# Kernel tuning notes

Measured on AMD Instinct MI355X. Metric: run time of the kernel, lower is better.

Reference implementation:

```python
import jax, jax.numpy as jnp
import numpy as np

N, E, CIN, H, L = 50000, 800000, 128, 256, 3
EPS = 1e-5  # BatchNorm1d default eps


def setup_inputs() -> dict:
    key = jax.random.key(0)
    ks = jax.random.split(key, 24)
    x = jax.random.normal(ks[0], (N, CIN), dtype=jnp.float32)
    edge_index = jax.random.randint(ks[1], (2, E), 0, N, dtype=jnp.int64)
    params = {}
    cin = CIN
    for i in range(L):
        s = 1.0 / np.sqrt(cin).astype(np.float32)
        params[f"Wl{i}"] = jax.random.normal(ks[2 + 3 * i], (cin, H), dtype=jnp.float32) * s
        params[f"Wr{i}"] = jax.random.normal(ks[3 + 3 * i], (cin, H), dtype=jnp.float32) * s
        params[f"b{i}"] = jax.random.normal(ks[4 + 3 * i], (H,), dtype=jnp.float32) * 0.01
        cin = H
    gamma = jax.random.uniform(ks[20], (L, H), minval=0.5, maxval=1.5, dtype=jnp.float32)
    beta = jax.random.normal(ks[21], (L, H), dtype=jnp.float32) * 0.1
    rmean = jax.random.normal(ks[22], (L, H), dtype=jnp.float32) * 0.1
    rvar = jax.random.uniform(ks[23], (L, H), minval=0.5, maxval=1.5, dtype=jnp.float32)
    return dict(x=x, edge_index=edge_index, gamma=gamma, beta=beta,
                rmean=rmean, rvar=rvar, **params)


def reference(x, edge_index, gamma, beta, rmean, rvar,
              Wl0, Wr0, b0, Wl1, Wr1, b1, Wl2, Wr2, b2):
    src, dst = edge_index[0], edge_index[1]
    # in-degree of each destination node, clamped to 1 (mean aggregation)
    deg = jnp.maximum(
        jax.ops.segment_sum(jnp.ones((E,), jnp.float32), dst, num_segments=N), 1.0
    )[:, None]

    def layer(h, Wl, Wr, b, g, bt, rm, rv):
        # SAGEConv (mean): out = lin_l(mean_j x_j) + lin_r(x)
        agg = jax.ops.segment_sum(h[src], dst, num_segments=N) / deg  # [N, C]
        out = agg @ Wl + h @ Wr + b                                   # [N, H]
        # BatchNorm1d (eval mode: running stats) + ReLU; dropout is identity in eval
        out = (out - rm) * jax.lax.rsqrt(rv + EPS) * g + bt
        return jax.nn.relu(out)

    weights = [(Wl0, Wr0, b0), (Wl1, Wr1, b1), (Wl2, Wr2, b2)]
    for i, (Wl, Wr, b) in enumerate(weights):
        x = layer(x, Wl, Wr, b, gamma[i], beta[i], rmean[i], rvar[i])
    return x
```

## Files before the change

kernel.cpp:

```cpp
#include <hip/hip_runtime.h>
#include <hip/hip_bf16.h>

#define NN 50000
#define PADN 50048
#define EE 800000
#define HH 256
#define EPSBN 1e-5f
#define NBLK ((NN + 255) / 256)

typedef unsigned int uint32;
typedef __attribute__((ext_vector_type(8))) short short8;
typedef __attribute__((ext_vector_type(4))) float f32x4;
typedef __attribute__((ext_vector_type(2))) float f32x2;

__device__ __forceinline__ float bf2f(unsigned short u) {
    union { uint32 u; float f; } c; c.u = ((uint32)u) << 16; return c.f;
}
__device__ __forceinline__ unsigned short f2bf(float f) {
    __hip_bfloat16 h = __float2bfloat16(f);
    return *reinterpret_cast<unsigned short*>(&h);
}
__device__ __forceinline__ uint32 pkfp8(float a, float b, float c, float d) {
    int r = 0;
    r = __builtin_amdgcn_cvt_pk_fp8_f32(a, b, r, false);
    r = __builtin_amdgcn_cvt_pk_fp8_f32(c, d, r, true);
    return (uint32)r;
}


__global__ void cvt_x(const float* __restrict__ x, unsigned short* __restrict__ xb,
                      unsigned char* __restrict__ x8, int* __restrict__ deg) {
    int i = blockIdx.x * blockDim.x + threadIdx.x;
    if (i < NN) deg[i] = 0;
    if (i >= PADN * 128 / 8) return;
    const int e0 = i * 8;
    float f[8];
    if (e0 + 8 <= NN * 128) {
        float4 u0 = *(const float4*)(x + e0);
        float4 u1 = *(const float4*)(x + e0 + 4);
        f[0] = u0.x; f[1] = u0.y; f[2] = u0.z; f[3] = u0.w;
        f[4] = u1.x; f[5] = u1.y; f[6] = u1.z; f[7] = u1.w;
    } else {
        #pragma unroll
        for (int k = 0; k < 8; ++k) f[k] = 0.f;
    }
    uint4 b;
    b.x = (uint32)f2bf(f[0]) | ((uint32)f2bf(f[1]) << 16);
    b.y = (uint32)f2bf(f[2]) | ((uint32)f2bf(f[3]) << 16);
    b.z = (uint32)f2bf(f[4]) | ((uint32)f2bf(f[5]) << 16);
    b.w = (uint32)f2bf(f[6]) | ((uint32)f2bf(f[7]) << 16);
    *(uint4*)(xb + e0) = b;
    uint2 p;
    p.x = pkfp8(f[0], f[1], f[2], f[3]);
    p.y = pkfp8(f[4], f[5], f[6], f[7]);
    *(uint2*)(x8 + e0) = p;
}

__global__ void count_rank(const int* __restrict__ dst, int* __restrict__ deg,
                           int* __restrict__ rank) {
    int e = blockIdx.x * blockDim.x + threadIdx.x;
    if (e < EE) rank[e] = atomicAdd(&deg[dst[e]], 1);
}

__global__ void scan_part(const int* __restrict__ deg, int* __restrict__ bsum) {
    __shared__ int sd[256];
    const int t = (int)threadIdx.x;
    const int i = (int)blockIdx.x * 256 + t;
    sd[t] = (i < NN) ? deg[i] : 0;
    __syncthreads();
    #pragma unroll
    for (int off = 128; off > 0; off >>= 1) {
        if (t < off) sd[t] += sd[t + off];
        __syncthreads();
    }
    if (t == 0) bsum[blockIdx.x] = sd[0];
}

__global__ void scan_fin(const int* __restrict__ deg, const int* __restrict__ bsum,
                         int* __restrict__ rowstart) {
    __shared__ int sb[256];
    __shared__ int sd[256];
    const int t = (int)threadIdx.x;
    const int b = (int)blockIdx.x;
    sb[t] = (t < NBLK && t < b) ? bsum[t] : 0;
    __syncthreads();
    #pragma unroll
    for (int off = 128; off > 0; off >>= 1) {
        if (t < off) sb[t] += sb[t + off];
        __syncthreads();
    }
    const int boff = sb[0];
    const int i = b * 256 + t;
    const int v = (i < NN) ? deg[i] : 0;
    sd[t] = v;
    __syncthreads();
    #pragma unroll
    for (int off = 1; off < 256; off <<= 1) {
        int u = (t >= off) ? sd[t - off] : 0;
        __syncthreads();
        sd[t] += u;
        __syncthreads();
    }
    if (i < NN) rowstart[i] = boff + sd[t] - v;
    if (i == 0) rowstart[NN] = EE;
}

__global__ void fill_csr2(const int* __restrict__ src, const int* __restrict__ dst,
                          const int* __restrict__ rank, const int* __restrict__ rowstart,
                          int* __restrict__ col) {
    int e = blockIdx.x * blockDim.x + threadIdx.x;
    if (e < EE) col[rowstart[dst[e]] + rank[e]] = src[e];
}

__device__ __forceinline__ void pack_one(const float* __restrict__ Wl,
                                         const float* __restrict__ Wr,
                                         unsigned short* __restrict__ Wp,
                                         int C, int idx) {
    int e  = idx & 7;
    int ll = (idx >> 3) & 63;
    int nf = (idx >> 9) & 15;
    int s  = idx >> 13;
    int KSl = C / 32;
    const float* W = (s < KSl) ? Wl : Wr;
    int ks = (s < KSl) ? s : s - KSl;
    int k = ks * 32 + (ll >> 4) * 8 + e;
    int n = nf * 16 + (ll & 15);
    Wp[idx] = f2bf(W[(size_t)k * HH + n]);
}

__global__ void pack_w3(const float* __restrict__ Wl0, const float* __restrict__ Wr0,
                        unsigned short* __restrict__ Wp0,
                        const float* __restrict__ Wl1, const float* __restrict__ Wr1,
                        unsigned short* __restrict__ Wp1,
                        const float* __restrict__ Wl2, const float* __restrict__ Wr2,
                        unsigned short* __restrict__ Wp2) {
    int idx = blockIdx.x * blockDim.x + threadIdx.x;
    if (idx < 65536)       pack_one(Wl0, Wr0, Wp0, 128, idx);
    else if (idx < 196608) pack_one(Wl1, Wr1, Wp1, 256, idx - 65536);
    else if (idx < 327680) pack_one(Wl2, Wr2, Wp2, 256, idx - 196608);
}


__device__ __forceinline__ void acc8f(float* a, uint2 v) {
    f32x2 f0 = __builtin_amdgcn_cvt_pk_f32_fp8(v.x, false);
    f32x2 f1 = __builtin_amdgcn_cvt_pk_f32_fp8(v.x, true);
    f32x2 f2 = __builtin_amdgcn_cvt_pk_f32_fp8(v.y, false);
    f32x2 f3 = __builtin_amdgcn_cvt_pk_f32_fp8(v.y, true);
    a[0] += f0.x; a[1] += f0.y; a[2] += f1.x; a[3] += f1.y;
    a[4] += f2.x; a[5] += f2.y; a[6] += f3.x; a[7] += f3.y;
}

template<int C>
__global__ void agg_mean_8(const unsigned char* __restrict__ h8, const int* __restrict__ rowstart,
                           const int* __restrict__ col,
                           unsigned short* __restrict__ agg) {
    const int wid = (int)((blockIdx.x * blockDim.x + threadIdx.x) >> 6);
    const int l   = (int)(threadIdx.x & 63);
    if (wid >= NN) return;
    const int beg = rowstart[wid], end = rowstart[wid + 1];
    const int d   = end - beg;
    const float inv = 1.0f / (float)(d > 1 ? d : 1);
    float a[8] = {0.f, 0.f, 0.f, 0.f, 0.f, 0.f, 0.f, 0.f};

    if (C == 256) {
        const int half = l >> 5;
        const int cl   = l & 31;
        const unsigned char* base = h8 + cl * 8;
        int j = beg + half;
        for (; j + 6 < end; j += 8) {
            int c0 = col[j], c1 = col[j + 2], c2 = col[j + 4], c3 = col[j + 6];
            uint2 v0 = *(const uint2*)(base + (size_t)c0 * C);
            uint2 v1 = *(const uint2*)(base + (size_t)c1 * C);
            uint2 v2 = *(const uint2*)(base + (size_t)c2 * C);
            uint2 v3 = *(const uint2*)(base + (size_t)c3 * C);
            acc8f(a, v0); acc8f(a, v1); acc8f(a, v2); acc8f(a, v3);
        }
        for (; j < end; j += 2) {
            uint2 v0 = *(const uint2*)(base + (size_t)col[j] * C);
            acc8f(a, v0);
        }
        #pragma unroll
        for (int k = 0; k < 8; ++k) a[k] += __shfl_xor(a[k], 32, 64);
        if (half == 0) {
            uint4 o;
            o.x = (uint32)f2bf(a[0] * inv) | ((uint32)f2bf(a[1] * inv) << 16);
            o.y = (uint32)f2bf(a[2] * inv) | ((uint32)f2bf(a[3] * inv) << 16);
            o.z = (uint32)f2bf(a[4] * inv) | ((uint32)f2bf(a[5] * inv) << 16);
            o.w = (uint32)f2bf(a[6] * inv) | ((uint32)f2bf(a[7] * inv) << 16);
            *(uint4*)(agg + (size_t)wid * C + cl * 8) = o;
        }
    } else {
        const int q  = l >> 4;
        const int cl = l & 15;
        const unsigned char* base = h8 + cl * 8;
        int j = beg + q;
        for (; j + 12 < end; j += 16) {
            int c0 = col[j], c1 = col[j + 4], c2 = col[j + 8], c3 = col[j + 12];
            uint2 v0 = *(const uint2*)(base + (size_t)c0 * C);
            uint2 v1 = *(const uint2*)(base + (size_t)c1 * C);
            uint2 v2 = *(const uint2*)(base + (size_t)c2 * C);
            uint2 v3 = *(const uint2*)(base + (size_t)c3 * C);
            acc8f(a, v0); acc8f(a, v1); acc8f(a, v2); acc8f(a, v3);
        }
        for (; j < end; j += 4) {
            uint2 v0 = *(const uint2*)(base + (size_t)col[j] * C);
            acc8f(a, v0);
        }
        #pragma unroll
        for (int k = 0; k < 8; ++k) {
            a[k] += __shfl_xor(a[k], 16, 64);
            a[k] += __shfl_xor(a[k], 32, 64);
        }
        if (q == 0) {
            uint4 o;
            o.x = (uint32)f2bf(a[0] * inv) | ((uint32)f2bf(a[1] * inv) << 16);
            o.y = (uint32)f2bf(a[2] * inv) | ((uint32)f2bf(a[3] * inv) << 16);
            o.z = (uint32)f2bf(a[4] * inv) | ((uint32)f2bf(a[5] * inv) << 16);
            o.w = (uint32)f2bf(a[6] * inv) | ((uint32)f2bf(a[7] * inv) << 16);
            *(uint4*)(agg + (size_t)wid * C + cl * 8) = o;
        }
    }
}


#define CPAD 260

template<int C, bool FINAL>
__global__ __launch_bounds__(256)
void gemm_mfma(const unsigned short* __restrict__ Aagg, const unsigned short* __restrict__ Ain,
               const unsigned short* __restrict__ Wpack,
               const float* __restrict__ bias, const float* __restrict__ gamma,
               const float* __restrict__ beta, const float* __restrict__ rmean,
               const float* __restrict__ rvar,
               float* __restrict__ outf, unsigned short* __restrict__ outb,
               unsigned char* __restrict__ out8)
{
    constexpr int KS = C / 32;
    constexpr int S  = 2 * KS;
    constexpr int NS = S / 2;
    __shared__ unsigned short Alds[2][4][1024];
    __shared__ __align__(16) unsigned char Cbuf[33280];
    const int tid = (int)threadIdx.x;
    const int wid = tid >> 6;
    const int l   = tid & 63;
    const int row0 = (int)blockIdx.x * 64;

    const int srow  = row0 + wid * 16 + (l & 15);
    const int skoff = (l >> 4) * 8;

    f32x4 acc[4][4];
    #pragma unroll
    for (int m = 0; m < 4; ++m)
        #pragma unroll
        for (int n = 0; n < 4; ++n)
            acc[m][n] = (f32x4){0.f, 0.f, 0.f, 0.f};

    auto stage = [&](int buf, int st) {
        #pragma unroll
        for (int k2 = 0; k2 < 2; ++k2) {
            const int s = st * 2 + k2;
            const unsigned short* Asrc = (s < KS) ? Aagg : Ain;
            const int ks = (s < KS) ? s : s - KS;
            const unsigned short* gp = Asrc + (size_t)srow * C + ks * 32 + skoff;
            __builtin_amdgcn_global_load_lds(
                (const __attribute__((address_space(1))) uint32*)gp,
                (__attribute__((address_space(3))) uint32*)(&Alds[buf][wid][k2 * 512]),
                16, 0, 0);
        }
    };

    stage(0, 0);
    int cur = 0;
    for (int st = 0; st < NS; ++st) {
        __syncthreads();
        if (st + 1 < NS) stage(cur ^ 1, st + 1);
        short8 b[2][4];
        #pragma unroll
        for (int k2 = 0; k2 < 2; ++k2)
            #pragma unroll
            for (int n = 0; n < 4; ++n) {
                size_t off = ((size_t)(st * 2 + k2) * 16 + wid * 4 + n) * 512 + l * 8;
                b[k2][n] = *(const short8*)(Wpack + off);
            }
        short8 a[2][4];
        #pragma unroll
        for (int k2 = 0; k2 < 2; ++k2)
            #pragma unroll
            for (int m = 0; m < 4; ++m)
                a[k2][m] = *(const short8*)(&Alds[cur][m][k2 * 512 + l * 8]);
        #pragma unroll
        for (int k2 = 0; k2 < 2; ++k2)
            #pragma unroll
            for (int m = 0; m < 4; ++m)
                #pragma unroll
                for (int n = 0; n < 4; ++n)
                    acc[m][n] = __builtin_amdgcn_mfma_f32_16x16x32_bf16(a[k2][m], b[k2][n], acc[m][n], 0, 0, 0);
        cur ^= 1;
    }

    float sj[4], cj[4];
    #pragma unroll
    for (int n = 0; n < 4; ++n) {
        const int jj = wid * 64 + n * 16 + (l & 15);
        sj[n] = gamma[jj] * rsqrtf(rvar[jj] + EPSBN);
        cj[n] = (bias[jj] - rmean[jj]) * sj[n] + beta[jj];
    }

    if (FINAL) {
        float* Cf = (float*)Cbuf;
        #pragma unroll
        for (int half = 0; half < 2; ++half) {
            if (half) __syncthreads();
            #pragma unroll
            for (int n = 0; n < 4; ++n) {
                const int jj = wid * 64 + n * 16 + (l & 15);
                #pragma unroll
                for (int mm = 0; mm < 2; ++mm) {
                    const int m  = half * 2 + mm;
                    const int rb = mm * 16 + (l >> 4) * 4;
                    #pragma unroll
                    for (int j = 0; j < 4; ++j) {
                        float v = acc[m][n][j] * sj[n] + cj[n];
                        Cf[(rb + j) * CPAD + jj] = v > 0.f ? v : 0.f;
                    }
                }
            }
            __syncthreads();
            const int col4 = (tid & 63) * 4;
            const int rw   = tid >> 6;
            #pragma unroll
            for (int i = 0; i < 8; ++i) {
                const int row  = i * 4 + rw;
                const int grow = row0 + half * 32 + row;
                if (grow < NN) {
                    float4 v = *(const float4*)&Cf[row * CPAD + col4];
                    *(float4*)(outf + (size_t)grow * HH + col4) = v;
                }
            }
        }
    } else {
        unsigned short* Clds = (unsigned short*)Cbuf;
        #pragma unroll
        for (int n = 0; n < 4; ++n) {
            const int jj = wid * 64 + n * 16 + (l & 15);
            #pragma unroll
            for (int m = 0; m < 4; ++m) {
                const int rb = m * 16 + (l >> 4) * 4;
                #pragma unroll
                for (int j = 0; j < 4; ++j) {
                    float v = acc[m][n][j] * sj[n] + cj[n];
                    Clds[(rb + j) * CPAD + jj] = f2bf(v > 0.f ? v : 0.f);
                }
            }
        }
        __syncthreads();
        #pragma unroll
        for (int i = 0; i < 8; ++i) {
            const int row  = i * 8 + (tid >> 5);
            const int col8 = (tid & 31) * 8;
            uint4 v = *(const uint4*)&Clds[row * CPAD + col8];
            *(uint4*)(outb + ((size_t)(row0 + row)) * HH + col8) = v;
            uint2 p;
            p.x = pkfp8(bf2f((unsigned short)(v.x & 0xffff)), bf2f((unsigned short)(v.x >> 16)),
                        bf2f((unsigned short)(v.y & 0xffff)), bf2f((unsigned short)(v.y >> 16)));
            p.y = pkfp8(bf2f((unsigned short)(v.z & 0xffff)), bf2f((unsigned short)(v.z >> 16)),
                        bf2f((unsigned short)(v.w & 0xffff)), bf2f((unsigned short)(v.w >> 16)));
            *(uint2*)(out8 + ((size_t)(row0 + row)) * HH + col8) = p;
        }
    }
}


static inline size_t alignup(size_t x) { return (x + 511) & ~(size_t)511; }

extern "C" void kernel_launch(void* const* d_in, const int* in_sizes, int n_in,
                              void* d_out, int out_size, void* d_ws, size_t ws_size,
                              hipStream_t stream) {
    const float* x   = (const float*)d_in[0];
    const int*   ei  = (const int*)d_in[1];
    const int*   src = ei;
    const int*   dst = ei + EE;
    const float* gamma = (const float*)d_in[2];
    const float* beta  = (const float*)d_in[3];
    const float* rmean = (const float*)d_in[4];
    const float* rvar  = (const float*)d_in[5];
    const float* Wl0 = (const float*)d_in[6];
    const float* Wr0 = (const float*)d_in[7];
    const float* b0  = (const float*)d_in[8];
    const float* Wl1 = (const float*)d_in[9];
    const float* Wr1 = (const float*)d_in[10];
    const float* b1  = (const float*)d_in[11];
    const float* Wl2 = (const float*)d_in[12];
    const float* Wr2 = (const float*)d_in[13];
    const float* b2  = (const float*)d_in[14];
    float* out = (float*)d_out;
    (void)ws_size; (void)n_in; (void)in_sizes; (void)out_size;

    char* w = (char*)d_ws;
    size_t off = 0;
    int*   deg      = (int*)(w + off);   off += alignup(NN * 4);
    int*   rank     = (int*)(w + off);   off += alignup((size_t)EE * 4);
    int*   rowstart = (int*)(w + off);   off += alignup((NN + 1) * 4);
    int*   bsum     = (int*)(w + off);   off += alignup(NBLK * 4);
    int*   col      = (int*)(w + off);   off += alignup((size_t)EE * 4);
    unsigned short* xb   = (unsigned short*)(w + off); off += alignup((size_t)PADN * 128 * 2);
    unsigned short* agg  = (unsigned short*)(w + off); off += alignup((size_t)PADN * HH * 2);
    unsigned short* h1   = (unsigned short*)(w + off); off += alignup((size_t)PADN * HH * 2);
    unsigned short* h2   = (unsigned short*)(w + off); off += alignup((size_t)PADN * HH * 2);
    unsigned char*  x8   = (unsigned char*)(w + off);  off += alignup((size_t)PADN * 128);
    unsigned char*  h1_8 = (unsigned char*)(w + off);  off += alignup((size_t)PADN * HH);
    unsigned char*  h2_8 = (unsigned char*)(w + off);  off += alignup((size_t)PADN * HH);
    unsigned short* Wp0  = (unsigned short*)(w + off); off += alignup((size_t)2 * 128 * 256 * 2);
    unsigned short* Wp1  = (unsigned short*)(w + off); off += alignup((size_t)2 * 256 * 256 * 2);
    unsigned short* Wp2  = (unsigned short*)(w + off); off += alignup((size_t)2 * 256 * 256 * 2);

    cvt_x     <<<(PADN * 128 / 8 + 255) / 256, 256, 0, stream>>>(x, xb, x8, deg);
    count_rank<<<(EE + 255) / 256, 256, 0, stream>>>(dst, deg, rank);
    scan_part <<<NBLK, 256, 0, stream>>>(deg, bsum);
    scan_fin  <<<NBLK, 256, 0, stream>>>(deg, bsum, rowstart);
    fill_csr2 <<<(EE + 255) / 256, 256, 0, stream>>>(src, dst, rank, rowstart, col);
    pack_w3   <<<1280, 256, 0, stream>>>(Wl0, Wr0, Wp0, Wl1, Wr1, Wp1, Wl2, Wr2, Wp2);

    const int agg_grid  = (NN * 64 + 255) / 256;
    const int gemm_grid = PADN / 64;

    agg_mean_8<128><<<agg_grid, 256, 0, stream>>>(x8, rowstart, col, agg);
    gemm_mfma<128, false><<<gemm_grid, 256, 0, stream>>>(agg, xb, Wp0,
        b0, gamma + 0 * HH, beta + 0 * HH, rmean + 0 * HH, rvar + 0 * HH, nullptr, h1, h1_8);

    agg_mean_8<256><<<agg_grid, 256, 0, stream>>>(h1_8, rowstart, col, agg);
    gemm_mfma<256, false><<<gemm_grid, 256, 0, stream>>>(agg, h1, Wp1,
        b1, gamma + 1 * HH, beta + 1 * HH, rmean + 1 * HH, rvar + 1 * HH, nullptr, h2, h2_8);

    agg_mean_8<256><<<agg_grid, 256, 0, stream>>>(h2_8, rowstart, col, agg);
    gemm_mfma<256, true><<<gemm_grid, 256, 0, stream>>>(agg, h2, Wp2,
        b2, gamma + 2 * HH, beta + 2 * HH, rmean + 2 * HH, rvar + 2 * HH, out, nullptr, nullptr);
}
```

Measured before the change: 329.1 us.

## Widen fp8 gather loads to 16 bytes and batch edges per thread in CSR build

The mean-aggregation kernel now has each lane load 16 fp8 features (uint4) per neighbour instead of 8. This lets more sub-warps process different neighbours in parallel, so there are more independent loads in flight, at the cost of 16 accumulators and an extra shuffle stage. The count_rank and fill_csr2 kernels now handle 8 and 4 edges per thread respectively, with a grid-stride layout, to expose more memory-level parallelism and issue fewer blocks. The extra register use could lower occupancy.

```diff
diff --git a/kernel.cpp b/kernel.cpp
--- a/kernel.cpp
+++ b/kernel.cpp
@@ -7,6 +7,8 @@
 #define HH 256
 #define EPSBN 1e-5f
 #define NBLK ((NN + 255) / 256)
+#define CR_T 100096
+#define FC_T 200192
 
 typedef unsigned int uint32;
 typedef __attribute__((ext_vector_type(8))) short short8;
@@ -58,8 +60,21 @@
 
 __global__ void count_rank(const int* __restrict__ dst, int* __restrict__ deg,
                            int* __restrict__ rank) {
-    int e = blockIdx.x * blockDim.x + threadIdx.x;
-    if (e < EE) rank[e] = atomicAdd(&deg[dst[e]], 1);
+    const int t = (int)(blockIdx.x * blockDim.x + threadIdx.x);
+    int d[8], r[8];
+    #pragma unroll
+    for (int k = 0; k < 8; ++k) {
+        const int e = t + k * CR_T;
+        d[k] = (e < EE) ? dst[e] : -1;
+    }
+    #pragma unroll
+    for (int k = 0; k < 8; ++k)
+        if (d[k] >= 0) r[k] = atomicAdd(&deg[d[k]], 1);
+    #pragma unroll
+    for (int k = 0; k < 8; ++k) {
+        const int e = t + k * CR_T;
+        if (d[k] >= 0) rank[e] = r[k];
+    }
 }
 
 __global__ void scan_part(const int* __restrict__ deg, int* __restrict__ bsum) {
@@ -108,8 +123,22 @@
 __global__ void fill_csr2(const int* __restrict__ src, const int* __restrict__ dst,
                           const int* __restrict__ rank, const int* __restrict__ rowstart,
                           int* __restrict__ col) {
-    int e = blockIdx.x * blockDim.x + threadIdx.x;
-    if (e < EE) col[rowstart[dst[e]] + rank[e]] = src[e];
+    const int t = (int)(blockIdx.x * blockDim.x + threadIdx.x);
+    int d[4], r[4], s[4], p[4];
+    #pragma unroll
+    for (int k = 0; k < 4; ++k) {
+        const int e = t + k * FC_T;
+        const bool ok = e < EE;
+        d[k] = ok ? dst[e] : -1;
+        r[k] = ok ? rank[e] : 0;
+        s[k] = ok ? src[e] : 0;
+    }
+    #pragma unroll
+    for (int k = 0; k < 4; ++k)
+        if (d[k] >= 0) p[k] = rowstart[d[k]];
+    #pragma unroll
+    for (int k = 0; k < 4; ++k)
+        if (d[k] >= 0) col[p[k] + r[k]] = s[k];
 }
 
 __device__ __forceinline__ void pack_one(const float* __restrict__ Wl,
@@ -141,13 +170,16 @@
 }
 
 
-__device__ __forceinline__ void acc8f(float* a, uint2 v) {
-    f32x2 f0 = __builtin_amdgcn_cvt_pk_f32_fp8(v.x, false);
-    f32x2 f1 = __builtin_amdgcn_cvt_pk_f32_fp8(v.x, true);
-    f32x2 f2 = __builtin_amdgcn_cvt_pk_f32_fp8(v.y, false);
-    f32x2 f3 = __builtin_amdgcn_cvt_pk_f32_fp8(v.y, true);
-    a[0] += f0.x; a[1] += f0.y; a[2] += f1.x; a[3] += f1.y;
-    a[4] += f2.x; a[5] += f2.y; a[6] += f3.x; a[7] += f3.y;
+__device__ __forceinline__ void acc16f(float* a, uint4 v) {
+    f32x2 t;
+    t = __builtin_amdgcn_cvt_pk_f32_fp8(v.x, false); a[0]  += t.x; a[1]  += t.y;
+    t = __builtin_amdgcn_cvt_pk_f32_fp8(v.x, true);  a[2]  += t.x; a[3]  += t.y;
+    t = __builtin_amdgcn_cvt_pk_f32_fp8(v.y, false); a[4]  += t.x; a[5]  += t.y;
+    t = __builtin_amdgcn_cvt_pk_f32_fp8(v.y, true);  a[6]  += t.x; a[7]  += t.y;
+    t = __builtin_amdgcn_cvt_pk_f32_fp8(v.z, false); a[8]  += t.x; a[9]  += t.y;
+    t = __builtin_amdgcn_cvt_pk_f32_fp8(v.z, true);  a[10] += t.x; a[11] += t.y;
+    t = __builtin_amdgcn_cvt_pk_f32_fp8(v.w, false); a[12] += t.x; a[13] += t.y;
+    t = __builtin_amdgcn_cvt_pk_f32_fp8(v.w, true);  a[14] += t.x; a[15] += t.y;
 }
 
 template<int C>
@@ -160,65 +192,50 @@
     const int beg = rowstart[wid], end = rowstart[wid + 1];
     const int d   = end - beg;
     const float inv = 1.0f / (float)(d > 1 ? d : 1);
-    float a[8] = {0.f, 0.f, 0.f, 0.f, 0.f, 0.f, 0.f, 0.f};
-
-    if (C == 256) {
-        const int half = l >> 5;
-        const int cl   = l & 31;
-        const unsigned char* base = h8 + cl * 8;
-        int j = beg + half;
-        for (; j + 6 < end; j += 8) {
-            int c0 = col[j], c1 = col[j + 2], c2 = col[j + 4], c3 = col[j + 6];
-            uint2 v0 = *(const uint2*)(base + (size_t)c0 * C);
-            uint2 v1 = *(const uint2*)(base + (size_t)c1 * C);
-            uint2 v2 = *(const uint2*)(base + (size_t)c2 * C);
-            uint2 v3 = *(const uint2*)(base + (size_t)c3 * C);
-            acc8f(a, v0); acc8f(a, v1); acc8f(a, v2); acc8f(a, v3);
-        }
-        for (; j < end; j += 2) {
-            uint2 v0 = *(const uint2*)(base + (size_t)col[j] * C);
-            acc8f(a, v0);
-        }
-        #pragma unroll
-        for (int k = 0; k < 8; ++k) a[k] += __shfl_xor(a[k], 32, 64);
-        if (half == 0) {
-            uint4 o;
-            o.x = (uint32)f2bf(a[0] * inv) | ((uint32)f2bf(a[1] * inv) << 16);
-            o.y = (uint32)f2bf(a[2] * inv) | ((uint32)f2bf(a[3] * inv) << 16);
-            o.z = (uint32)f2bf(a[4] * inv) | ((uint32)f2bf(a[5] * inv) << 16);
-            o.w = (uint32)f2bf(a[6] * inv) | ((uint32)f2bf(a[7] * inv) << 16);
-            *(uint4*)(agg + (size_t)wid * C + cl * 8) = o;
-        }
-    } else {
-        const int q  = l >> 4;
-        const int cl = l & 15;
-        const unsigned char* base = h8 + cl * 8;
-        int j = beg + q;
-        for (; j + 12 < end; j += 16) {
-            int c0 = col[j], c1 = col[j + 4], c2 = col[j + 8], c3 = col[j + 12];
-            uint2 v0 = *(const uint2*)(base + (size_t)c0 * C);
-            uint2 v1 = *(const uint2*)(base + (size_t)c1 * C);
-            uint2 v2 = *(const uint2*)(base + (size_t)c2 * C);
-            uint2 v3 = *(const uint2*)(base + (size_t)c3 * C);
-            acc8f(a, v0); acc8f(a, v1); acc8f(a, v2); acc8f(a, v3);
-        }
-        for (; j < end; j += 4) {
-            uint2 v0 = *(const uint2*)(base + (size_t)col[j] * C);
-            acc8f(a, v0);
-        }
-        #pragma unroll
-        for (int k = 0; k < 8; ++k) {
-            a[k] += __shfl_xor(a[k], 16, 64);
-            a[k] += __shfl_xor(a[k], 32, 64);
-        }
-        if (q == 0) {
-            uint4 o;
-            o.x = (uint32)f2bf(a[0] * inv) | ((uint32)f2bf(a[1] * inv) << 16);
-            o.y = (uint32)f2bf(a[2] * inv) | ((uint32)f2bf(a[3] * inv) << 16);
-            o.z = (uint32)f2bf(a[4] * inv) | ((uint32)f2bf(a[5] * inv) << 16);
-            o.w = (uint32)f2bf(a[6] * inv) | ((uint32)f2bf(a[7] * inv) << 16);
-            *(uint4*)(agg + (size_t)wid * C + cl * 8) = o;
-        }
+    float a[16];
+    #pragma unroll
+    for (int k = 0; k < 16; ++k) a[k] = 0.f;
+
+    constexpr int LPR  = C / 16;
+    constexpr int NSW  = 64 / LPR;
+    const int sw = l / LPR;
+    const int cl = l % LPR;
+    const unsigned char* base = h8 + cl * 16;
+
+    int j = beg + sw;
+    for (; j + 3 * NSW < end; j += 4 * NSW) {
+        int c0 = col[j], c1 = col[j + NSW], c2 = col[j + 2 * NSW], c3 = col[j + 3 * NSW];
+        uint4 v0 = *(const uint4*)(base + (size_t)c0 * C);
+        uint4 v1 = *(const uint4*)(base + (size_t)c1 * C);
+        uint4 v2 = *(const uint4*)(base + (size_t)c2 * C);
+        uint4 v3 = *(const uint4*)(base + (size_t)c3 * C);
+        acc16f(a, v0); acc16f(a, v1); acc16f(a, v2); acc16f(a, v3);
+    }
+    for (; j < end; j += NSW) {
+        uint4 v0 = *(const uint4*)(base + (size_t)col[j] * C);
+        acc16f(a, v0);
+    }
+    if (C == 128) {
+        #pragma unroll
+        for (int k = 0; k < 16; ++k) a[k] += __shfl_xor(a[k], 8, 64);
+    }
+    #pragma unroll
+    for (int k = 0; k < 16; ++k) {
+        a[k] += __shfl_xor(a[k], 16, 64);
+        a[k] += __shfl_xor(a[k], 32, 64);
+    }
+    if (sw == 0) {
+        uint4 o0, o1;
+        o0.x = (uint32)f2bf(a[0]  * inv) | ((uint32)f2bf(a[1]  * inv) << 16);
+        o0.y = (uint32)f2bf(a[2]  * inv) | ((uint32)f2bf(a[3]  * inv) << 16);
+        o0.z = (uint32)f2bf(a[4]  * inv) | ((uint32)f2bf(a[5]  * inv) << 16);
+        o0.w = (uint32)f2bf(a[6]  * inv) | ((uint32)f2bf(a[7]  * inv) << 16);
+        o1.x = (uint32)f2bf(a[8]  * inv) | ((uint32)f2bf(a[9]  * inv) << 16);
+        o1.y = (uint32)f2bf(a[10] * inv) | ((uint32)f2bf(a[11] * inv) << 16);
+        o1.z = (uint32)f2bf(a[12] * inv) | ((uint32)f2bf(a[13] * inv) << 16);
+        o1.w = (uint32)f2bf(a[14] * inv) | ((uint32)f2bf(a[15] * inv) << 16);
+        *(uint4*)(agg + (size_t)wid * C + cl * 16) = o0;
+        *(uint4*)(agg + (size_t)wid * C + cl * 16 + 8) = o1;
     }
 }
 
@@ -415,10 +432,10 @@
     unsigned short* Wp2  = (unsigned short*)(w + off); off += alignup((size_t)2 * 256 * 256 * 2);
 
     cvt_x     <<<(PADN * 128 / 8 + 255) / 256, 256, 0, stream>>>(x, xb, x8, deg);
-    count_rank<<<(EE + 255) / 256, 256, 0, stream>>>(dst, deg, rank);
+    count_rank<<<CR_T / 256, 256, 0, stream>>>(dst, deg, rank);
     scan_part <<<NBLK, 256, 0, stream>>>(deg, bsum);
     scan_fin  <<<NBLK, 256, 0, stream>>>(deg, bsum, rowstart);
-    fill_csr2 <<<(EE + 255) / 256, 256, 0, stream>>>(src, dst, rank, rowstart, col);
+    fill_csr2 <<<FC_T / 256, 256, 0, stream>>>(src, dst, rank, rowstart, col);
     pack_w3   <<<1280, 256, 0, stream>>>(Wl0, Wr0, Wp0, Wl1, Wr1, Wp1, Wl2, Wr2, Wp2);
 
     const int agg_grid  = (NN * 64 + 255) / 256;
```

After: 357.8 us. 8.7% more time.
